# Kernel tuning notes

Measured on AMD Instinct MI355X. Metric: run time of the kernel, lower is better.

## Reference

```python
import jax, jax.numpy as jnp
import numpy as np
from jax import lax


def _maxpool_nchw(x, k):
    # Non-overlapping kxk max pool over the last two dims (NCHW).
    return lax.reduce_window(x, -jnp.inf, lax.max,
                             window_dimensions=(1, 1, k, k),
                             window_strides=(1, 1, k, k),
                             padding='VALID')


def setup_inputs() -> dict:
    key = jax.random.key(0)
    k1, k2, k3, k4, k5 = jax.random.split(key, 5)
    B = 16
    return {
        'input_tensor1': jax.random.normal(k1, (B, 128, 48, 48), jnp.float32),
        'input_tensor2': jax.random.normal(k2, (B, 64, 96, 96), jnp.float32),
        'input_tensor3': jax.random.normal(k3, (B, 32, 192, 192), jnp.float32),
        'input_tensor4': jax.random.normal(k4, (B, 16, 384, 384), jnp.float32),
        'pure_ff': jax.random.normal(k5, (B, 256, 24, 24), jnp.float32),
    }


def reference(input_tensor1, input_tensor2, input_tensor3, input_tensor4, pure_ff):
    # and then max-pools. Pooling is per-channel, so this equals pooling once
    # and tiling the pooled result along the channel axis -- same math,
    # without materializing the redundant concat intermediates.
    x1 = jnp.tile(_maxpool_nchw(input_tensor1, 2), (1, 2, 1, 1))   # [B,256,24,24]
    x2 = jnp.tile(_maxpool_nchw(input_tensor2, 4), (1, 4, 1, 1))   # [B,256,24,24]
    x3 = jnp.tile(_maxpool_nchw(input_tensor3, 8), (1, 8, 1, 1))   # [B,256,24,24]
    x4 = jnp.tile(_maxpool_nchw(input_tensor4, 16), (1, 16, 1, 1)) # [B,256,24,24]
    return jax.nn.relu(x1 + x2 + x3 + x4 + pure_ff)
```

## Files before the change

### kernel.cpp

```cpp
#include <hip/hip_runtime.h>
#include <math.h>


namespace {

constexpr int BATCH = 16;
constexpr int OHW   = 24;
constexpr int PLANE = OHW * OHW;

template <int K>
__device__ __forceinline__ float pool_window(const float* __restrict__ p, int stride) {
  float m = -INFINITY;
  if constexpr (K == 2) {
#pragma unroll
    for (int r = 0; r < 2; ++r) {
      float2 v = *reinterpret_cast<const float2*>(p + r * stride);
      m = fmaxf(m, fmaxf(v.x, v.y));
    }
  } else {
#pragma unroll
    for (int r = 0; r < K; ++r) {
#pragma unroll
      for (int c = 0; c < K; c += 4) {
        float4 v = *reinterpret_cast<const float4*>(p + r * stride + c);
        m = fmaxf(m, fmaxf(fmaxf(v.x, v.y), fmaxf(v.z, v.w)));
      }
    }
  }
  return m;
}

template <int K, int C>
__global__ __launch_bounds__(256) void pool_kernel(const float* __restrict__ in,
                                                   float* __restrict__ out) {
  constexpr int W     = OHW * K;
  constexpr int total = BATCH * C * PLANE;
  const int idx = blockIdx.x * 256 + threadIdx.x;
  if (idx >= total) return;
  const int ow = idx % OHW;
  const int oh = (idx / OHW) % OHW;
  const int bc = idx / PLANE;
  const float* p = in + (size_t)bc * (W * W) + (size_t)(oh * K) * W + ow * K;
  out[idx] = pool_window<K>(p, W);
}

__global__ __launch_bounds__(256) void combine_kernel(const float* __restrict__ p1,
                                                      const float* __restrict__ p2,
                                                      const float* __restrict__ p3,
                                                      const float* __restrict__ p4,
                                                      const float* __restrict__ ff,
                                                      float* __restrict__ out) {
  constexpr int total4 = BATCH * 256 * PLANE / 4;
  const int idx = blockIdx.x * 256 + threadIdx.x;
  if (idx >= total4) return;
  const int hw4 = idx % (PLANE / 4);
  const int c   = (idx / (PLANE / 4)) % 256;
  const int b   = idx / ((PLANE / 4) * 256);
  const int hw  = hw4 * 4;

  const float4 a1 = *reinterpret_cast<const float4*>(p1 + (size_t)(b * 128 + (c & 127)) * PLANE + hw);
  const float4 a2 = *reinterpret_cast<const float4*>(p2 + (size_t)(b * 64  + (c & 63 )) * PLANE + hw);
  const float4 a3 = *reinterpret_cast<const float4*>(p3 + (size_t)(b * 32  + (c & 31 )) * PLANE + hw);
  const float4 a4 = *reinterpret_cast<const float4*>(p4 + (size_t)(b * 16  + (c & 15 )) * PLANE + hw);
  const float4 f  = *reinterpret_cast<const float4*>(ff + (size_t)idx * 4);

  float4 r;
  r.x = fmaxf((((a1.x + a2.x) + a3.x) + a4.x) + f.x, 0.0f);
  r.y = fmaxf((((a1.y + a2.y) + a3.y) + a4.y) + f.y, 0.0f);
  r.z = fmaxf((((a1.z + a2.z) + a3.z) + a4.z) + f.z, 0.0f);
  r.w = fmaxf((((a1.w + a2.w) + a3.w) + a4.w) + f.w, 0.0f);
  *reinterpret_cast<float4*>(out + (size_t)idx * 4) = r;
}

__global__ __launch_bounds__(256) void fused_naive(const float* __restrict__ x1,
                                                   const float* __restrict__ x2,
                                                   const float* __restrict__ x3,
                                                   const float* __restrict__ x4,
                                                   const float* __restrict__ ff,
                                                   float* __restrict__ out) {
  constexpr int total = BATCH * 256 * PLANE;
  const int idx = blockIdx.x * 256 + threadIdx.x;
  if (idx >= total) return;
  const int hw = idx % PLANE;
  const int w  = hw % OHW;
  const int h  = hw / OHW;
  const int c  = (idx / PLANE) % 256;
  const int b  = idx / (PLANE * 256);

  float s = pool_window<2>(x1 + (size_t)(b * 128 + (c & 127)) * (48 * 48)   + (size_t)(h * 2)  * 48  + w * 2,  48);
  s = s + pool_window<4>( x2 + (size_t)(b * 64  + (c & 63 )) * (96 * 96)   + (size_t)(h * 4)  * 96  + w * 4,  96);
  s = s + pool_window<8>( x3 + (size_t)(b * 32  + (c & 31 )) * (192 * 192) + (size_t)(h * 8)  * 192 + w * 8,  192);
  s = s + pool_window<16>(x4 + (size_t)(b * 16  + (c & 15 )) * (384 * 384) + (size_t)(h * 16) * 384 + w * 16, 384);
  s = s + ff[idx];
  out[idx] = fmaxf(s, 0.0f);
}

}

extern "C" void kernel_launch(void* const* d_in, const int* in_sizes, int n_in,
                              void* d_out, int out_size, void* d_ws, size_t ws_size,
                              hipStream_t stream) {
  const float* x1 = (const float*)d_in[0];
  const float* x2 = (const float*)d_in[1];
  const float* x3 = (const float*)d_in[2];
  const float* x4 = (const float*)d_in[3];
  const float* ff = (const float*)d_in[4];
  float* out = (float*)d_out;

  constexpr size_t n1 = (size_t)BATCH * 128 * PLANE;
  constexpr size_t n2 = (size_t)BATCH * 64  * PLANE;
  constexpr size_t n3 = (size_t)BATCH * 32  * PLANE;
  constexpr size_t n4 = (size_t)BATCH * 16  * PLANE;
  constexpr size_t need = (n1 + n2 + n3 + n4) * sizeof(float);

  if (ws_size >= need) {
    float* p1 = (float*)d_ws;
    float* p2 = p1 + n1;
    float* p3 = p2 + n2;
    float* p4 = p3 + n3;
    pool_kernel<2, 128><<<n1 / 256, 256, 0, stream>>>(x1, p1);
    pool_kernel<4, 64 ><<<n2 / 256, 256, 0, stream>>>(x2, p2);
    pool_kernel<8, 32 ><<<n3 / 256, 256, 0, stream>>>(x3, p3);
    pool_kernel<16, 16><<<n4 / 256, 256, 0, stream>>>(x4, p4);
    constexpr int total4 = BATCH * 256 * PLANE / 4;
    combine_kernel<<<total4 / 256, 256, 0, stream>>>(p1, p2, p3, p4, ff, out);
  } else {
    constexpr int total = BATCH * 256 * PLANE;
    fused_naive<<<(total + 255) / 256, 256, 0, stream>>>(x1, x2, x3, x4, ff, out);
  }
}
```

Measured before the change: 323.8 us.

## Fuse all pooling and combine into one row-tiled block kernel with shared memory

Replaces four pooling kernels plus a combine kernel with a single kernel where each block handles one batch, output row and half-row. Pooled values for all channels are staged in shared memory, with coalesced float4 loads and shuffle reductions for wide windows, then broadcast across channels with ff added. This removes workspace round-trips and extra launches, but the grid is small (768 blocks), which may limit latency hiding.

```diff
diff --git a/kernel.cpp b/kernel.cpp
--- a/kernel.cpp
+++ b/kernel.cpp
@@ -4,95 +4,114 @@
 
 namespace {
 
-constexpr int BATCH = 16;
-constexpr int OHW   = 24;
-constexpr int PLANE = OHW * OHW;
+constexpr int OHW = 24;
 
-template <int K>
-__device__ __forceinline__ float pool_window(const float* __restrict__ p, int stride) {
-  float m = -INFINITY;
-  if constexpr (K == 2) {
+__device__ __forceinline__ float fmax4(const float4 v) {
+  return fmaxf(fmaxf(v.x, v.y), fmaxf(v.z, v.w));
+}
+
+__global__ __launch_bounds__(256, 3) void fused_block(const float* __restrict__ x1,
+                                                      const float* __restrict__ x2,
+                                                      const float* __restrict__ x3,
+                                                      const float* __restrict__ x4,
+                                                      const float* __restrict__ ff,
+                                                      float* __restrict__ out) {
+  __shared__ __attribute__((aligned(16))) float s1[128 * 12];
+  __shared__ __attribute__((aligned(16))) float s2[64 * 12];
+  __shared__ __attribute__((aligned(16))) float s3[32 * 12];
+  __shared__ __attribute__((aligned(16))) float s4[16 * 12];
+
+  const int blk  = blockIdx.x;
+  const int b    = blk / 48;
+  const int rem  = blk % 48;
+  const int oh   = rem >> 1;
+  const int half = rem & 1;
+  const int tid  = threadIdx.x;
+
+  {
+    const float* base = x1 + (size_t)b * 128 * 2304 + oh * 2 * 48 + half * 24;
 #pragma unroll
-    for (int r = 0; r < 2; ++r) {
-      float2 v = *reinterpret_cast<const float2*>(p + r * stride);
-      m = fmaxf(m, fmaxf(v.x, v.y));
-    }
-  } else {
-#pragma unroll
-    for (int r = 0; r < K; ++r) {
-#pragma unroll
-      for (int c = 0; c < K; c += 4) {
-        float4 v = *reinterpret_cast<const float4*>(p + r * stride + c);
-        m = fmaxf(m, fmaxf(fmaxf(v.x, v.y), fmaxf(v.z, v.w)));
-      }
+    for (int it = 0; it < 3; ++it) {
+      const int t  = it * 256 + tid;
+      const int ch = t / 6, pid = t % 6;
+      const float* p = base + (size_t)ch * 2304 + pid * 4;
+      const float4 a = *reinterpret_cast<const float4*>(p);
+      const float4 c = *reinterpret_cast<const float4*>(p + 48);
+      s1[ch * 12 + pid * 2]     = fmaxf(fmaxf(a.x, a.y), fmaxf(c.x, c.y));
+      s1[ch * 12 + pid * 2 + 1] = fmaxf(fmaxf(a.z, a.w), fmaxf(c.z, c.w));
     }
   }
-  return m;
-}
 
-template <int K, int C>
-__global__ __launch_bounds__(256) void pool_kernel(const float* __restrict__ in,
-                                                   float* __restrict__ out) {
-  constexpr int W     = OHW * K;
-  constexpr int total = BATCH * C * PLANE;
-  const int idx = blockIdx.x * 256 + threadIdx.x;
-  if (idx >= total) return;
-  const int ow = idx % OHW;
-  const int oh = (idx / OHW) % OHW;
-  const int bc = idx / PLANE;
-  const float* p = in + (size_t)bc * (W * W) + (size_t)(oh * K) * W + ow * K;
-  out[idx] = pool_window<K>(p, W);
-}
+  {
+    const float* base = x2 + (size_t)b * 64 * 9216 + oh * 4 * 96 + half * 48;
+#pragma unroll
+    for (int it = 0; it < 3; ++it) {
+      const int t  = it * 256 + tid;
+      const int ch = t / 12, ow = t % 12;
+      const float* p = base + (size_t)ch * 9216 + ow * 4;
+      float m = -INFINITY;
+#pragma unroll
+      for (int r = 0; r < 4; ++r)
+        m = fmaxf(m, fmax4(*reinterpret_cast<const float4*>(p + r * 96)));
+      s2[ch * 12 + ow] = m;
+    }
+  }
 
-__global__ __launch_bounds__(256) void combine_kernel(const float* __restrict__ p1,
-                                                      const float* __restrict__ p2,
-                                                      const float* __restrict__ p3,
-                                                      const float* __restrict__ p4,
-                                                      const float* __restrict__ ff,
-                                                      float* __restrict__ out) {
-  constexpr int total4 = BATCH * 256 * PLANE / 4;
-  const int idx = blockIdx.x * 256 + threadIdx.x;
-  if (idx >= total4) return;
-  const int hw4 = idx % (PLANE / 4);
-  const int c   = (idx / (PLANE / 4)) % 256;
-  const int b   = idx / ((PLANE / 4) * 256);
-  const int hw  = hw4 * 4;
+  {
+    const float* base = x3 + (size_t)b * 32 * 36864 + oh * 8 * 192 + half * 96;
+#pragma unroll
+    for (int it = 0; it < 3; ++it) {
+      const int t  = it * 256 + tid;
+      const int ch = t / 24, ow = (t % 24) >> 1, hf = t & 1;
+      const float* p = base + (size_t)ch * 36864 + ow * 8 + hf * 4;
+      float m = -INFINITY;
+#pragma unroll
+      for (int r = 0; r < 8; ++r)
+        m = fmaxf(m, fmax4(*reinterpret_cast<const float4*>(p + r * 192)));
+      m = fmaxf(m, __shfl_xor(m, 1));
+      if (hf == 0) s3[ch * 12 + ow] = m;
+    }
+  }
 
-  const float4 a1 = *reinterpret_cast<const float4*>(p1 + (size_t)(b * 128 + (c & 127)) * PLANE + hw);
-  const float4 a2 = *reinterpret_cast<const float4*>(p2 + (size_t)(b * 64  + (c & 63 )) * PLANE + hw);
-  const float4 a3 = *reinterpret_cast<const float4*>(p3 + (size_t)(b * 32  + (c & 31 )) * PLANE + hw);
-  const float4 a4 = *reinterpret_cast<const float4*>(p4 + (size_t)(b * 16  + (c & 15 )) * PLANE + hw);
-  const float4 f  = *reinterpret_cast<const float4*>(ff + (size_t)idx * 4);
+  {
+    const float* base = x4 + (size_t)b * 16 * 147456 + oh * 16 * 384 + half * 192;
+#pragma unroll
+    for (int it = 0; it < 3; ++it) {
+      const int t  = it * 256 + tid;
+      const int ch = t / 48, ow = (t % 48) >> 2, q = t & 3;
+      const float* p = base + (size_t)ch * 147456 + ow * 16 + q * 4;
+      float m = -INFINITY;
+#pragma unroll
+      for (int r = 0; r < 16; ++r)
+        m = fmaxf(m, fmax4(*reinterpret_cast<const float4*>(p + r * 384)));
+      m = fmaxf(m, __shfl_xor(m, 1));
+      m = fmaxf(m, __shfl_xor(m, 2));
+      if (q == 0) s4[ch * 12 + ow] = m;
+    }
+  }
 
-  float4 r;
-  r.x = fmaxf((((a1.x + a2.x) + a3.x) + a4.x) + f.x, 0.0f);
-  r.y = fmaxf((((a1.y + a2.y) + a3.y) + a4.y) + f.y, 0.0f);
-  r.z = fmaxf((((a1.z + a2.z) + a3.z) + a4.z) + f.z, 0.0f);
-  r.w = fmaxf((((a1.w + a2.w) + a3.w) + a4.w) + f.w, 0.0f);
-  *reinterpret_cast<float4*>(out + (size_t)idx * 4) = r;
-}
+  __syncthreads();
 
-__global__ __launch_bounds__(256) void fused_naive(const float* __restrict__ x1,
-                                                   const float* __restrict__ x2,
-                                                   const float* __restrict__ x3,
-                                                   const float* __restrict__ x4,
-                                                   const float* __restrict__ ff,
-                                                   float* __restrict__ out) {
-  constexpr int total = BATCH * 256 * PLANE;
-  const int idx = blockIdx.x * 256 + threadIdx.x;
-  if (idx >= total) return;
-  const int hw = idx % PLANE;
-  const int w  = hw % OHW;
-  const int h  = hw / OHW;
-  const int c  = (idx / PLANE) % 256;
-  const int b  = idx / (PLANE * 256);
-
-  float s = pool_window<2>(x1 + (size_t)(b * 128 + (c & 127)) * (48 * 48)   + (size_t)(h * 2)  * 48  + w * 2,  48);
-  s = s + pool_window<4>( x2 + (size_t)(b * 64  + (c & 63 )) * (96 * 96)   + (size_t)(h * 4)  * 96  + w * 4,  96);
-  s = s + pool_window<8>( x3 + (size_t)(b * 32  + (c & 31 )) * (192 * 192) + (size_t)(h * 8)  * 192 + w * 8,  192);
-  s = s + pool_window<16>(x4 + (size_t)(b * 16  + (c & 15 )) * (384 * 384) + (size_t)(h * 16) * 384 + w * 16, 384);
-  s = s + ff[idx];
-  out[idx] = fmaxf(s, 0.0f);
+  {
+    const size_t obase = (size_t)b * 256 * 576 + oh * OHW + half * 12;
+#pragma unroll
+    for (int it = 0; it < 3; ++it) {
+      const int t = it * 256 + tid;
+      const int c = t / 3, q = (t % 3) * 4;
+      const float4 a1 = *reinterpret_cast<const float4*>(&s1[(c & 127) * 12 + q]);
+      const float4 a2 = *reinterpret_cast<const float4*>(&s2[(c & 63)  * 12 + q]);
+      const float4 a3 = *reinterpret_cast<const float4*>(&s3[(c & 31)  * 12 + q]);
+      const float4 a4 = *reinterpret_cast<const float4*>(&s4[(c & 15)  * 12 + q]);
+      const size_t o  = obase + (size_t)c * 576 + q;
+      const float4 f  = *reinterpret_cast<const float4*>(ff + o);
+      float4 r;
+      r.x = fmaxf((((a1.x + a2.x) + a3.x) + a4.x) + f.x, 0.0f);
+      r.y = fmaxf((((a1.y + a2.y) + a3.y) + a4.y) + f.y, 0.0f);
+      r.z = fmaxf((((a1.z + a2.z) + a3.z) + a4.z) + f.z, 0.0f);
+      r.w = fmaxf((((a1.w + a2.w) + a3.w) + a4.w) + f.w, 0.0f);
+      *reinterpret_cast<float4*>(out + o) = r;
+    }
+  }
 }
 
 }
@@ -106,26 +125,7 @@
   const float* x4 = (const float*)d_in[3];
   const float* ff = (const float*)d_in[4];
   float* out = (float*)d_out;
+  (void)d_ws; (void)ws_size; (void)in_sizes; (void)n_in; (void)out_size;
 
-  constexpr size_t n1 = (size_t)BATCH * 128 * PLANE;
-  constexpr size_t n2 = (size_t)BATCH * 64  * PLANE;
-  constexpr size_t n3 = (size_t)BATCH * 32  * PLANE;
-  constexpr size_t n4 = (size_t)BATCH * 16  * PLANE;
-  constexpr size_t need = (n1 + n2 + n3 + n4) * sizeof(float);
-
-  if (ws_size >= need) {
-    float* p1 = (float*)d_ws;
-    float* p2 = p1 + n1;
-    float* p3 = p2 + n2;
-    float* p4 = p3 + n3;
-    pool_kernel<2, 128><<<n1 / 256, 256, 0, stream>>>(x1, p1);
-    pool_kernel<4, 64 ><<<n2 / 256, 256, 0, stream>>>(x2, p2);
-    pool_kernel<8, 32 ><<<n3 / 256, 256, 0, stream>>>(x3, p3);
-    pool_kernel<16, 16><<<n4 / 256, 256, 0, stream>>>(x4, p4);
-    constexpr int total4 = BATCH * 256 * PLANE / 4;
-    combine_kernel<<<total4 / 256, 256, 0, stream>>>(p1, p2, p3, p4, ff, out);
-  } else {
-    constexpr int total = BATCH * 256 * PLANE;
-    fused_naive<<<(total + 255) / 256, 256, 0, stream>>>(x1, x2, x3, x4, ff, out);
-  }
+  fused_block<<<768, 256, 0, stream>>>(x1, x2, x3, x4, ff, out);
 }
```

New measurement: 314.3 us. 1.03x faster.
